# Kernel tuning notes

Hardware: AMD Instinct MI355X
Metric: run time of the kernel (lower is better)

## Reference

```python
import jax, jax.numpy as jnp
import numpy as np
from jax import lax

SR = 4      # sr_ratio
HEADS = 8   # num_heads


def _upsample_bilinear_ac(x, out_h, out_w):
    # torch nn.Upsample(scale_factor=SR, mode='bilinear', align_corners=True)
    B, C, h, w = x.shape
    ys = jnp.linspace(0.0, h - 1.0, out_h)
    xs = jnp.linspace(0.0, w - 1.0, out_w)
    y0 = jnp.floor(ys).astype(jnp.int32)
    y1 = jnp.minimum(y0 + 1, h - 1)
    wy = (ys - y0).astype(x.dtype)
    x0 = jnp.floor(xs).astype(jnp.int32)
    x1 = jnp.minimum(x0 + 1, w - 1)
    wx = (xs - x0).astype(x.dtype)
    r = x[:, :, y0, :] * (1.0 - wy)[None, None, :, None] + x[:, :, y1, :] * wy[None, None, :, None]
    return r[:, :, :, x0] * (1.0 - wx) + r[:, :, :, x1] * wx


def _forward(x, sr_w, sr_b, ln_g, ln_b, q_w, k1_w, v1_w, k2_w, v2_w, proj_w, proj_b):
    B, C, H, W = x.shape
    ID = C // 4                      # internal_dim
    hd = ID // HEADS                 # head_dim
    scale = float(hd) ** -0.5
    # spatial-reduction conv for Q path: [B, ID, H/4, W/4]
    qf = lax.conv_general_dilated(x, sr_w, (SR, SR), 'VALID',
                                  dimension_numbers=('NCHW', 'OIHW', 'NCHW'))
    qf = qf + sr_b[None, :, None, None]
    Hs, Ws = qf.shape[2], qf.shape[3]
    N = Hs * Ws
    qf = qf.reshape(B, ID, N).transpose(0, 2, 1)          # [B, N, ID]
    # LayerNorm
    mu = qf.mean(-1, keepdims=True)
    var = qf.var(-1, keepdims=True)
    qn = (qf - mu) / jnp.sqrt(var + 1e-5) * ln_g + ln_b
    q = qn @ q_w                                          # [B, N, ID]
    # max / avg pooled K,V inputs: [B, N, C]
    xm = lax.reduce_window(x, -jnp.inf, lax.max, (1, 1, SR, SR), (1, 1, SR, SR), 'VALID')
    xm = xm.reshape(B, C, N).transpose(0, 2, 1)
    xa = lax.reduce_window(x, 0.0, lax.add, (1, 1, SR, SR), (1, 1, SR, SR), 'VALID') / float(SR * SR)
    xa = xa.reshape(B, C, N).transpose(0, 2, 1)

    def heads(t):
        return t.reshape(B, N, HEADS, hd).transpose(0, 2, 1, 3)  # [B, H, N, hd]

    qh = heads(q)
    k1, v1 = heads(xm @ k1_w), heads(xm @ v1_w)
    k2, v2 = heads(xa @ k2_w), heads(xa @ v2_w)

    def attend(k, v):
        a = jax.nn.softmax(jnp.einsum('bhnd,bhmd->bhnm', qh, k) * scale, axis=-1)
        return jnp.einsum('bhnm,bhmd->bhnd', a, v)

    z = attend(k1, v1) + attend(k2, v2)                   # [B, H, N, hd]
    z = z.transpose(0, 2, 1, 3).reshape(B, N, ID)
    z = z @ proj_w + proj_b                               # [B, N, C]
    z = z.transpose(0, 2, 1).reshape(B, C, Hs, Ws)
    return _upsample_bilinear_ac(z, H, W)


def setup_inputs() -> dict:
    key = jax.random.key(0)
    ks = jax.random.split(key, 9)
    B, C, H, W = 16, 256, 112, 112
    ID = C // 4

    def n(k, shape, s=0.02):
        return jax.random.normal(k, shape, jnp.float32) * s

    return {
        'x': jax.random.normal(ks[0], (B, C, H, W), jnp.float32),
        'sr_w': n(ks[1], (ID, C, SR, SR)),
        'sr_b': jnp.zeros((ID,), jnp.float32),
        'ln_g': jnp.ones((ID,), jnp.float32),
        'ln_b': jnp.zeros((ID,), jnp.float32),
        'q_w': n(ks[2], (ID, ID)),
        'k1_w': n(ks[3], (C, ID)),
        'v1_w': n(ks[4], (C, ID)),
        'k2_w': n(ks[5], (C, ID)),
        'v2_w': n(ks[6], (C, ID)),
        'proj_w': n(ks[7], (ID, C)),
        'proj_b': jnp.zeros((C,), jnp.float32),
    }


def reference(x, sr_w, sr_b, ln_g, ln_b, q_w, k1_w, v1_w, k2_w, v2_w, proj_w, proj_b):
    return _forward(x, sr_w, sr_b, ln_g, ln_b, q_w, k1_w, v1_w, k2_w, v2_w, proj_w, proj_b)
```

## Files before the change

kernel.cpp:

```cpp
#include <hip/hip_runtime.h>
#include <math.h>

typedef __attribute__((ext_vector_type(8))) short short8;
typedef __attribute__((ext_vector_type(4))) short bh4;
typedef __attribute__((ext_vector_type(4))) float f32x4;
typedef __attribute__((ext_vector_type(2))) unsigned uint2v;
typedef __attribute__((ext_vector_type(4))) unsigned uint4v;

#define MFMA16(A,B,C) __builtin_amdgcn_mfma_f32_16x16x32_bf16(A,B,C,0,0,0)

#if __has_builtin(__builtin_amdgcn_mfma_f32_16x16x16bf16_1k)
#define MFMA16x16(A,B,C) __builtin_amdgcn_mfma_f32_16x16x16bf16_1k(A,B,C,0,0,0)
#else
__device__ __forceinline__ f32x4 mfma16x16_asm(bh4 a, bh4 b, f32x4 c){
    asm volatile("v_mfma_f32_16x16x16_bf16 %0, %1, %2, %0" : "+v"(c) : "v"(a), "v"(b));
    return c;
}
#define MFMA16x16(A,B,C) mfma16x16_asm(A,B,C)
#endif

__device__ __forceinline__ unsigned short f2b(float f){
    unsigned u = __builtin_bit_cast(unsigned, f);
    return (unsigned short)((u + 0x7fffu + ((u>>16)&1u)) >> 16);
}
__device__ __forceinline__ unsigned pk2(float a, float b){
    return (unsigned)f2b(a) | ((unsigned)f2b(b) << 16);
}
__device__ __forceinline__ unsigned pk2rn(float a, float b){
    unsigned ua = __builtin_bit_cast(unsigned, a) + 0x8000u;
    unsigned ub = __builtin_bit_cast(unsigned, b) + 0x8000u;
    return (ua >> 16) | (ub & 0xffff0000u);
}


__global__ __launch_bounds__(256) void ktw(const float* __restrict__ srw,
    const float* __restrict__ qw, const float* __restrict__ k1w,
    const float* __restrict__ v1w, const float* __restrict__ k2w,
    const float* __restrict__ v2w, char* __restrict__ srwb,
    char* __restrict__ Wtm, char* __restrict__ Wta, char* __restrict__ QWt)
{
    int blk = blockIdx.x, t = threadIdx.x;
    if (blk < 128){
        int base = blk*2048 + t*8;
        float4 a = *(const float4*)(srw + base);
        float4 b = *(const float4*)(srw + base + 4);
        uint4 u = { pk2(a.x,a.y), pk2(a.z,a.w), pk2(b.x,b.y), pk2(b.z,b.w) };
        *(uint4*)(srwb + (size_t)base*2) = u;
    } else if (blk < 136){
        __shared__ float T[256*33];
        int idx = blk - 128, fi = idx >> 1, half = idx & 1;
        const float* src = (fi==0) ? k1w : (fi==1) ? v1w : (fi==2) ? k2w : v2w;
        char* dst = ((fi < 2) ? Wtm : Wta) + (size_t)((fi & 1)*64 + half*32) * 512;
        for (int li = t; li < 8192; li += 256){
            int c = li >> 5, o = li & 31;
            T[c*33 + o] = src[c*64 + half*32 + o];
        }
        __syncthreads();
        for (int lo = t; lo < 1024; lo += 256){
            int o = lo >> 5, c8 = lo & 31;
            float v[8];
            #pragma unroll
            for (int k = 0; k < 8; ++k) v[k] = T[(c8*8 + k)*33 + o];
            uint4 u = { pk2(v[0],v[1]), pk2(v[2],v[3]), pk2(v[4],v[5]), pk2(v[6],v[7]) };
            *(uint4*)(dst + o*512 + c8*16) = u;
        }
    } else {
        __shared__ float T[64*65];
        for (int li = t; li < 4096; li += 256)
            T[(li >> 6)*65 + (li & 63)] = qw[li];
        __syncthreads();
        for (int lo = t; lo < 512; lo += 256){
            int o = lo >> 3, i8 = lo & 7;
            float v[8];
            #pragma unroll
            for (int k = 0; k < 8; ++k) v[k] = T[(i8*8 + k)*65 + o];
            uint4 u = { pk2(v[0],v[1]), pk2(v[2],v[3]), pk2(v[4],v[5]), pk2(v[6],v[7]) };
            *(uint4*)(QWt + o*128 + i8*16) = u;
        }
    }
}

__global__ __launch_bounds__(256) void k1(const float* __restrict__ x,
    const char* __restrict__ srwb, char* __restrict__ R, float* __restrict__ pws)
{
    __shared__ float pm[28*66];
    __shared__ float pa[28*66];
    int blk = blockIdx.x;
    int b = blk / 112, r5 = blk % 112, hs = r5 >> 2, cg4 = r5 & 3;
    int t = threadIdx.x;
    int w = t >> 6, l = t & 63, lr = l & 15, lg = l >> 4;
    int cpar = lg >> 1, r0 = (lg & 1) * 2;
    f32x4 acc0 = {0.f,0.f,0.f,0.f}, acc1 = {0.f,0.f,0.f,0.f};
    const float* xc = x + (size_t)(b*256 + cg4*64)*12544 + (size_t)(hs*4 + r0)*112;
    const char* Brow = srwb + (size_t)(w*16 + lr)*8192 + cg4*2048 + lg*16;
    int p0 = lr, p1 = min(16 + lr, 27);
    size_t rowB = (size_t)b*784 + hs*28;

    #pragma unroll 8
    for (int ks = 0; ks < 32; ++ks){
        const float* s = xc + (size_t)(ks*2 + cpar)*12544;
        float4 a0r0 = *(const float4*)(s + p0*4);
        float4 a0r1 = *(const float4*)(s + 112 + p0*4);
        float4 a1r0 = *(const float4*)(s + p1*4);
        float4 a1r1 = *(const float4*)(s + 112 + p1*4);
        short8 bf = *(const short8*)(Brow + ks*64);
        if (w == 0){
            float mx0 = fmaxf(fmaxf(fmaxf(a0r0.x,a0r0.y),fmaxf(a0r0.z,a0r0.w)),
                              fmaxf(fmaxf(a0r1.x,a0r1.y),fmaxf(a0r1.z,a0r1.w)));
            float sm0 = (a0r0.x+a0r0.y)+(a0r0.z+a0r0.w)+(a0r1.x+a0r1.y)+(a0r1.z+a0r1.w);
            float mx1 = fmaxf(fmaxf(fmaxf(a1r0.x,a1r0.y),fmaxf(a1r0.z,a1r0.w)),
                              fmaxf(fmaxf(a1r1.x,a1r1.y),fmaxf(a1r1.z,a1r1.w)));
            float sm1 = (a1r0.x+a1r0.y)+(a1r0.z+a1r0.w)+(a1r1.x+a1r1.y)+(a1r1.z+a1r1.w);
            mx0 = fmaxf(mx0, __shfl_xor(mx0, 16, 64));
            sm0 = sm0 + __shfl_xor(sm0, 16, 64);
            mx1 = fmaxf(mx1, __shfl_xor(mx1, 16, 64));
            sm1 = sm1 + __shfl_xor(sm1, 16, 64);
            if ((lg & 1) == 0){
                int c = ks*2 + cpar;
                pm[p0*66 + c] = mx0; pa[p0*66 + c] = sm0 * (1.f/16.f);
                if (lr < 12){ pm[p1*66 + c] = mx1; pa[p1*66 + c] = sm1 * (1.f/16.f); }
            }
        }
        short8 af0 = __builtin_bit_cast(short8,
            (uint4v){ pk2(a0r0.x,a0r0.y), pk2(a0r0.z,a0r0.w), pk2(a0r1.x,a0r1.y), pk2(a0r1.z,a0r1.w) });
        short8 af1 = __builtin_bit_cast(short8,
            (uint4v){ pk2(a1r0.x,a1r0.y), pk2(a1r0.z,a1r0.w), pk2(a1r1.x,a1r1.y), pk2(a1r1.z,a1r1.w) });
        acc0 = MFMA16(af0, bf, acc0);
        acc1 = MFMA16(af1, bf, acc1);
    }

    float* pp = pws + (size_t)((b*28 + hs)*4 + cg4)*1792;
    #pragma unroll
    for (int rg = 0; rg < 4; ++rg){
        int m0 = lg*4 + rg, m1 = 16 + lg*4 + rg;
        pp[m0*64 + w*16 + lr] = acc0[rg];
        if (m1 < 28) pp[m1*64 + w*16 + lr] = acc1[rg];
    }
    __syncthreads();
    if (t < 224){
        int m = t >> 3, sub = t & 7;
        float vm[8], va8[8];
        #pragma unroll
        for (int k = 0; k < 8; ++k){
            vm[k]  = pm[m*66 + sub*8 + k];
            va8[k] = pa[m*66 + sub*8 + k];
        }
        uint4 um = { pk2(vm[0],vm[1]), pk2(vm[2],vm[3]), pk2(vm[4],vm[5]), pk2(vm[6],vm[7]) };
        uint4 ua = { pk2(va8[0],va8[1]), pk2(va8[2],va8[3]), pk2(va8[4],va8[5]), pk2(va8[6],va8[7]) };
        *(uint4*)(R + (rowB + m)*1024 + cg4*128 + sub*16)       = um;
        *(uint4*)(R + (rowB + m)*1024 + 512 + cg4*128 + sub*16) = ua;
    }
}

__global__ __launch_bounds__(512) void k2(const float* __restrict__ pws_,
    const float* __restrict__ srb, const float* __restrict__ lng,
    const float* __restrict__ lnb, const char* __restrict__ Wtm,
    const char* __restrict__ Wta, const char* __restrict__ QWt,
    char* __restrict__ R)
{
    __shared__ __align__(16) char PM[16384];
    __shared__ __align__(16) char PA[16384];
    __shared__ float Db[32*64];
    __shared__ __align__(16) char QN[4096];
    int blk = blockIdx.x, b = blk/28, hs = blk%28;
    int t = threadIdx.x, w = t>>6, l = t&63, lr = l&15, lg = l>>4;
    size_t rowB = (size_t)b*784 + hs*28;
    const char* Rb = R + rowB*1024;
    for (int li = t; li < 896; li += 512){
        int m = li >> 5, c16 = li & 31;
        uint4 vm = *(const uint4*)(Rb + (size_t)m*1024 + c16*16);
        uint4 va = *(const uint4*)(Rb + (size_t)m*1024 + 512 + c16*16);
        int dst = m*512 + ((c16*16) ^ ((m&7)<<4));
        *(uint4*)(PM + dst) = vm;
        *(uint4*)(PA + dst) = va;
    }
    const float* p0 = pws_ + (size_t)(b*28 + hs)*4*1792;
    for (int e = t; e < 1792; e += 512)
        Db[e] = ((p0[e] + p0[1792+e]) + (p0[3584+e] + p0[5376+e])) + srb[e & 63];
    __syncthreads();
    float g = lng[l], be = lnb[l];
    #pragma unroll
    for (int i = 0; i < 4; ++i){
        int m = w + i*8;
        float v = Db[m*64 + l];
        float s = v, ss = v*v;
        #pragma unroll
        for (int off = 1; off < 64; off <<= 1){
            s  += __shfl_xor(s,  off, 64);
            ss += __shfl_xor(ss, off, 64);
        }
        float mu = s * (1.f/64.f);
        float var = ss * (1.f/64.f) - mu*mu;
        float qn = (v - mu) * rsqrtf(var + 1e-5f) * g + be;
        *(unsigned short*)(QN + m*128 + ((l*2) ^ ((m&7)<<4))) = f2b(qn);
    }
    __syncthreads();
    int fam = w >> 2, ofp = w & 3;
    const char* PMA = fam ? PA : PM;
    const char* Wt  = fam ? Wta : Wtm;
    f32x4 a00={0.f,0.f,0.f,0.f}, a01=a00, a10=a00, a11=a00;
    int swzr = (lr & 7) << 4;
    #pragma unroll
    for (int ks = 0; ks < 8; ++ks){
        int kb = ks*64 + lg*16;
        short8 x0 = *(const short8*)(PMA + lr*512 + (kb ^ swzr));
        short8 x1 = *(const short8*)(PMA + (16+lr)*512 + (kb ^ swzr));
        short8 b0 = *(const short8*)(Wt + (size_t)(ofp*32 + lr)*512 + kb);
        short8 b1 = *(const short8*)(Wt + (size_t)(ofp*32 + 16 + lr)*512 + kb);
        a00 = MFMA16(x0, b0, a00); a01 = MFMA16(x0, b1, a01);
        a10 = MFMA16(x1, b0, a10); a11 = MFMA16(x1, b1, a11);
    }
    f32x4 q0={0.f,0.f,0.f,0.f}, q1=q0;
    if (w < 4){
        #pragma unroll
        for (int ks = 0; ks < 2; ++ks){
            int kb = ks*64 + lg*16;
            short8 xa_ = *(const short8*)(QN + lr*128 + (kb ^ swzr));
            short8 xb_ = *(const short8*)(QN + (16+lr)*128 + (kb ^ swzr));
            short8 bq  = *(const short8*)(QWt + (size_t)(w*16 + lr)*128 + kb);
            q0 = MFMA16(xa_, bq, q0);
            q1 = MFMA16(xb_, bq, q1);
        }
    }
    #pragma unroll
    for (int j = 0; j < 2; ++j){
        int o128 = ofp*32 + j*16 + lr;
        int o = o128 & 63, hh = o >> 3, dd = o & 7, mat = fam*2 + (o128 >> 6);
        int byteoff = 128 + hh*64 + mat*16 + dd*2;
        f32x4 am  = j ? a01 : a00;
        f32x4 am1 = j ? a11 : a10;
        #pragma unroll
        for (int rg = 0; rg < 4; ++rg){
            int m0 = lg*4 + rg, m1 = 16 + lg*4 + rg;
            *(unsigned short*)(R + (rowB + m0)*1024 + byteoff) = f2b(am[rg]);
            if (m1 < 28)
                *(unsigned short*)(R + (rowB + m1)*1024 + byteoff) = f2b(am1[rg]);
        }
    }
    if (w < 4){
        int o = w*16 + lr;
        #pragma unroll
        for (int rg = 0; rg < 4; ++rg){
            int m0 = lg*4 + rg, m1 = 16 + lg*4 + rg;
            *(unsigned short*)(R + (rowB + m0)*1024 + o*2) = f2b(q0[rg]);
            if (m1 < 28)
                *(unsigned short*)(R + (rowB + m1)*1024 + o*2) = f2b(q1[rg]);
        }
    }
}

__global__ __launch_bounds__(256) void kattn(const char* __restrict__ R, float* __restrict__ z)
{
    __shared__ __align__(16) char QT [6144];
    __shared__ __align__(16) char K1b[5376];
    __shared__ __align__(16) char K2b[5376];
    __shared__ __align__(16) char VT1[3840];
    __shared__ __align__(16) char VT2[3840];
    int blk = blockIdx.x;
    int bh = blk / 7, nseg = blk % 7;
    int b = bh >> 3, h = bh & 7;
    int t = threadIdx.x, w = t >> 6, l = t & 63;
    int col = l & 15, g = l >> 4;

    for (int i = t; i < 384; i += 256) ((uint4*)QT)[i] = uint4{0,0,0,0};
    for (int i = t; i < 112; i += 256){
        *(uint4*)(K1b + i*48 + 16) = uint4{0,0,0,0};
        *(uint4*)(K2b + i*48 + 16) = uint4{0,0,0,0};
    }
    for (int i = t; i < 120; i += 256){
        *(uint4*)(VT1 + 1920 + i*16) = uint4{0,0,0,0};
        *(uint4*)(VT2 + 1920 + i*16) = uint4{0,0,0,0};
    }
    __syncthreads();
    if (t < 112){
        uint4 qv = *(const uint4*)(R + ((size_t)b*784 + nseg*112 + t)*1024 + h*16);
        *(uint2*)(QT + t*48)     = uint2{qv.x, qv.y};
        *(uint2*)(QT + t*48 + 8) = uint2{qv.z, qv.w};
    }
    __syncthreads();

    bh4 qf[2];
    #pragma unroll
    for (int nf = 0; nf < 2; ++nf)
        qf[nf] = *(const bh4*)(QT + (w*28 + nf*16 + col)*48 + g*8);

    f32x4 o1[2] = {{0,0,0,0},{0,0,0,0}}, o2[2] = {{0,0,0,0},{0,0,0,0}};
    float d1[2] = {0.f,0.f}, d2[2] = {0.f,0.f};
    const float C2 = 0.51004244f;

    for (int mt = 0; mt < 7; ++mt){
        __syncthreads();
        for (int li = t; li < 448; li += 256){
            int m = li >> 2, part = li & 3;
            uint4 v = *(const uint4*)(R + ((size_t)b*784 + mt*112 + m)*1024 + 128 + h*64 + part*16);
            if ((part & 1) == 0){
                char* Kb = (part == 0) ? K1b : K2b;
                *(uint2*)(Kb + m*48)     = uint2{v.x, v.y};
                *(uint2*)(Kb + m*48 + 8) = uint2{v.z, v.w};
            } else {
                char* Vb = (part == 1) ? VT1 : VT2;
                unsigned arr[4] = {v.x, v.y, v.z, v.w};
                #pragma unroll
                for (int d = 0; d < 4; ++d){
                    *(unsigned short*)(Vb + (d*2)*240   + m*2) = (unsigned short)(arr[d] & 0xffffu);
                    *(unsigned short*)(Vb + (d*2+1)*240 + m*2) = (unsigned short)(arr[d] >> 16);
                }
            }
        }
        __syncthreads();
        #pragma unroll
        for (int mc = 0; mc < 7; ++mc){
            bh4 ka = *(const bh4*)(K1b + (mc*16 + col)*48 + g*8);
            bh4 kb = *(const bh4*)(K2b + (mc*16 + col)*48 + g*8);
            bh4 va = *(const bh4*)(VT1 + col*240 + mc*32 + g*8);
            bh4 vb = *(const bh4*)(VT2 + col*240 + mc*32 + g*8);
            #pragma unroll
            for (int nf = 0; nf < 2; ++nf){
                f32x4 zr = {0.f,0.f,0.f,0.f};
                f32x4 s1 = MFMA16x16(ka, qf[nf], zr);
                float p0 = exp2f(s1[0]*C2), p1 = exp2f(s1[1]*C2);
                float p2 = exp2f(s1[2]*C2), p3 = exp2f(s1[3]*C2);
                d1[nf] += (p0+p1)+(p2+p3);
                bh4 pf1 = __builtin_bit_cast(bh4, (uint2v){pk2rn(p0,p1), pk2rn(p2,p3)});
                o1[nf] = MFMA16x16(va, pf1, o1[nf]);
                f32x4 s2 = MFMA16x16(kb, qf[nf], zr);
                float r0 = exp2f(s2[0]*C2), r1 = exp2f(s2[1]*C2);
                float r2 = exp2f(s2[2]*C2), r3 = exp2f(s2[3]*C2);
                d2[nf] += (r0+r1)+(r2+r3);
                bh4 pf2 = __builtin_bit_cast(bh4, (uint2v){pk2rn(r0,r1), pk2rn(r2,r3)});
                o2[nf] = MFMA16x16(vb, pf2, o2[nf]);
            }
        }
    }
    #pragma unroll
    for (int nf = 0; nf < 2; ++nf){
        d1[nf] += __shfl_xor(d1[nf], 16, 64); d1[nf] += __shfl_xor(d1[nf], 32, 64);
        d2[nf] += __shfl_xor(d2[nf], 16, 64); d2[nf] += __shfl_xor(d2[nf], 32, 64);
    }
    if (g < 2){
        #pragma unroll
        for (int nf = 0; nf < 2; ++nf){
            if (nf == 1 && col >= 12) continue;
            int n = nseg*112 + w*28 + nf*16 + col;
            float ra = 1.f / d1[nf], rb = 1.f / d2[nf];
            float4 ov;
            ov.x = o1[nf][0]*ra + o2[nf][0]*rb;
            ov.y = o1[nf][1]*ra + o2[nf][1]*rb;
            ov.z = o1[nf][2]*ra + o2[nf][2]*rb;
            ov.w = o1[nf][3]*ra + o2[nf][3]*rb;
            *(float4*)(z + ((size_t)b*784 + n)*64 + h*8 + g*4) = ov;
        }
    }
}

__global__ __launch_bounds__(256) void kproj(const float* __restrict__ z,
    const float* __restrict__ pw, const float* __restrict__ pb,
    float* __restrict__ zc)
{
    __shared__ float zs[28*64];
    int blk = blockIdx.x;
    int b = blk / 28, hs = blk % 28;
    int t = threadIdx.x;
    const float* zrow = z + ((size_t)b*784 + hs*28)*64;
    for (int li = t; li < 1792; li += 256) zs[li] = zrow[li];
    __syncthreads();
    int c = t;
    float acc[28];
    float bias = pb[c];
    #pragma unroll
    for (int wsI = 0; wsI < 28; ++wsI) acc[wsI] = bias;
    for (int o = 0; o < 64; ++o){
        float wv = pw[o*256 + c];
        #pragma unroll
        for (int wsI = 0; wsI < 28; ++wsI) acc[wsI] = fmaf(zs[wsI*64+o], wv, acc[wsI]);
    }
    float* op = zc + (((size_t)(b*256 + c))*28 + hs)*28;
    #pragma unroll
    for (int f = 0; f < 7; ++f)
        ((float4*)op)[f] = make_float4(acc[4*f], acc[4*f+1], acc[4*f+2], acc[4*f+3]);
}

__global__ __launch_bounds__(256) void kups(const float* __restrict__ zc, float* __restrict__ out)
{
    __shared__ float plane[784];
    __shared__ int   ti0[112];
    __shared__ float twv[112];
    int bc = blockIdx.x;
    int t = threadIdx.x;
    const float* src = zc + (size_t)bc*784;
    for (int li = t; li < 784; li += 256) plane[li] = src[li];
    if (t < 112){
        float s = (float)t * (27.f/111.f);
        int i0 = (int)s;
        if (i0 > 27) i0 = 27;
        ti0[t] = i0;
        twv[t] = s - (float)i0;
    }
    __syncthreads();
    float* op = out + (size_t)bc*12544;
    for (int i = t; i < 12544; i += 256){
        int y = i/112, xx = i%112;
        int y0 = ti0[y], x0 = ti0[xx];
        float wy = twv[y], wx = twv[xx];
        int y1 = min(y0+1, 27), x1 = min(x0+1, 27);
        const float* r0 = plane + y0*28;
        const float* r1 = plane + y1*28;
        float a  = r0[x0] + (r1[x0]-r0[x0])*wy;
        float bb = r0[x1] + (r1[x1]-r0[x1])*wy;
        op[i] = a + (bb-a)*wx;
    }
}

extern "C" void kernel_launch(void* const* d_in, const int* in_sizes, int n_in,
                              void* d_out, int out_size, void* d_ws, size_t ws_size,
                              hipStream_t stream) {
    const float* x   = (const float*)d_in[0];
    const float* srw = (const float*)d_in[1];
    const float* srb = (const float*)d_in[2];
    const float* lng = (const float*)d_in[3];
    const float* lnb = (const float*)d_in[4];
    const float* qw  = (const float*)d_in[5];
    const float* k1w = (const float*)d_in[6];
    const float* v1w = (const float*)d_in[7];
    const float* k2w = (const float*)d_in[8];
    const float* v2w = (const float*)d_in[9];
    const float* pw  = (const float*)d_in[10];
    const float* pb  = (const float*)d_in[11];

    char*  Rws  = (char*)d_ws;
    float* pws  = (float*)(Rws + 12845056);
    char*  srwb = Rws + 25690112;
    char*  Wtm  = Rws + 26214400;
    char*  Wta  = Rws + 26279936;
    char*  QWt  = Rws + 26345472;
    float* z    = (float*)(Rws + 12845056);
    float* zc   = (float*)(Rws + 16056320);
    float* out  = (float*)d_out;

    ktw  <<<137,  256, 0, stream>>>(srw, qw, k1w, v1w, k2w, v2w, srwb, Wtm, Wta, QWt);
    k1   <<<1792, 256, 0, stream>>>(x, srwb, Rws, pws);
    k2   <<<448,  512, 0, stream>>>(pws, srb, lng, lnb, Wtm, Wta, QWt, Rws);
    kattn<<<896,  256, 0, stream>>>(Rws, z);
    kproj<<<448,  256, 0, stream>>>(z, pw, pb, zc);
    kups <<<4096, 256, 0, stream>>>(zc, out);
}
```

Before: 284.4 us.

## Fuse projection with bilinear upsample and software-pipeline k1 loads

Merges the output projection and the bilinear upsample into one kernel. Each block computes 8 channel planes of one batch in shared memory and upsamples them directly to the output, so the intermediate zc buffer is never written to or read back from global memory. Separately, k1's channel loop is double-buffered by hand, loading the next two channel pairs while processing the current ones, and gets a launch-bounds occupancy hint. The cost is more registers in k1 and only 512 blocks for the fused kernel, each of which re-reads z.

```diff
diff --git a/kernel.cpp b/kernel.cpp
--- a/kernel.cpp
+++ b/kernel.cpp
@@ -80,7 +80,7 @@
     }
 }
 
-__global__ __launch_bounds__(256) void k1(const float* __restrict__ x,
+__global__ __launch_bounds__(256, 4) void k1(const float* __restrict__ x,
     const char* __restrict__ srwb, char* __restrict__ R, float* __restrict__ pws)
 {
     __shared__ float pm[28*66];
@@ -96,38 +96,56 @@
     int p0 = lr, p1 = min(16 + lr, 27);
     size_t rowB = (size_t)b*784 + hs*28;
 
-    #pragma unroll 8
-    for (int ks = 0; ks < 32; ++ks){
-        const float* s = xc + (size_t)(ks*2 + cpar)*12544;
-        float4 a0r0 = *(const float4*)(s + p0*4);
-        float4 a0r1 = *(const float4*)(s + 112 + p0*4);
-        float4 a1r0 = *(const float4*)(s + p1*4);
-        float4 a1r1 = *(const float4*)(s + 112 + p1*4);
-        short8 bf = *(const short8*)(Brow + ks*64);
-        if (w == 0){
-            float mx0 = fmaxf(fmaxf(fmaxf(a0r0.x,a0r0.y),fmaxf(a0r0.z,a0r0.w)),
-                              fmaxf(fmaxf(a0r1.x,a0r1.y),fmaxf(a0r1.z,a0r1.w)));
-            float sm0 = (a0r0.x+a0r0.y)+(a0r0.z+a0r0.w)+(a0r1.x+a0r1.y)+(a0r1.z+a0r1.w);
-            float mx1 = fmaxf(fmaxf(fmaxf(a1r0.x,a1r0.y),fmaxf(a1r0.z,a1r0.w)),
-                              fmaxf(fmaxf(a1r1.x,a1r1.y),fmaxf(a1r1.z,a1r1.w)));
-            float sm1 = (a1r0.x+a1r0.y)+(a1r0.z+a1r0.w)+(a1r1.x+a1r1.y)+(a1r1.z+a1r1.w);
-            mx0 = fmaxf(mx0, __shfl_xor(mx0, 16, 64));
-            sm0 = sm0 + __shfl_xor(sm0, 16, 64);
-            mx1 = fmaxf(mx1, __shfl_xor(mx1, 16, 64));
-            sm1 = sm1 + __shfl_xor(sm1, 16, 64);
-            if ((lg & 1) == 0){
-                int c = ks*2 + cpar;
-                pm[p0*66 + c] = mx0; pa[p0*66 + c] = sm0 * (1.f/16.f);
-                if (lr < 12){ pm[p1*66 + c] = mx1; pa[p1*66 + c] = sm1 * (1.f/16.f); }
-            }
-        }
-        short8 af0 = __builtin_bit_cast(short8,
-            (uint4v){ pk2(a0r0.x,a0r0.y), pk2(a0r0.z,a0r0.w), pk2(a0r1.x,a0r1.y), pk2(a0r1.z,a0r1.w) });
-        short8 af1 = __builtin_bit_cast(short8,
-            (uint4v){ pk2(a1r0.x,a1r0.y), pk2(a1r0.z,a1r0.w), pk2(a1r1.x,a1r1.y), pk2(a1r1.z,a1r1.w) });
-        acc0 = MFMA16(af0, bf, acc0);
-        acc1 = MFMA16(af1, bf, acc1);
-    }
+    float4 XA0,XA1,XA2,XA3,XA4,XA5,XA6,XA7; short8 BA0,BA1;
+    float4 XB0,XB1,XB2,XB3,XB4,XB5,XB6,XB7; short8 BB0,BB1;
+
+#define LD2(X0,X1,X2,X3,X4,X5,X6,X7,Bq0,Bq1,KS) do{ \
+    const float* _s0 = xc + (size_t)((KS)*2 + cpar)*12544; \
+    const float* _s1 = xc + (size_t)(((KS)+1)*2 + cpar)*12544; \
+    X0=*(const float4*)(_s0+p0*4); X1=*(const float4*)(_s0+112+p0*4); \
+    X2=*(const float4*)(_s0+p1*4); X3=*(const float4*)(_s0+112+p1*4); \
+    X4=*(const float4*)(_s1+p0*4); X5=*(const float4*)(_s1+112+p0*4); \
+    X6=*(const float4*)(_s1+p1*4); X7=*(const float4*)(_s1+112+p1*4); \
+    Bq0=*(const short8*)(Brow+(KS)*64); Bq1=*(const short8*)(Brow+((KS)+1)*64); }while(0)
+
+#define PROC1(Y0,Y1,Y2,Y3,BF,KS) do{ \
+    if (w == 0){ \
+        float mx0 = fmaxf(fmaxf(fmaxf(Y0.x,Y0.y),fmaxf(Y0.z,Y0.w)), \
+                          fmaxf(fmaxf(Y1.x,Y1.y),fmaxf(Y1.z,Y1.w))); \
+        float sm0 = (Y0.x+Y0.y)+(Y0.z+Y0.w)+(Y1.x+Y1.y)+(Y1.z+Y1.w); \
+        float mx1 = fmaxf(fmaxf(fmaxf(Y2.x,Y2.y),fmaxf(Y2.z,Y2.w)), \
+                          fmaxf(fmaxf(Y3.x,Y3.y),fmaxf(Y3.z,Y3.w))); \
+        float sm1 = (Y2.x+Y2.y)+(Y2.z+Y2.w)+(Y3.x+Y3.y)+(Y3.z+Y3.w); \
+        mx0 = fmaxf(mx0, __shfl_xor(mx0, 16, 64)); \
+        sm0 = sm0 + __shfl_xor(sm0, 16, 64); \
+        mx1 = fmaxf(mx1, __shfl_xor(mx1, 16, 64)); \
+        sm1 = sm1 + __shfl_xor(sm1, 16, 64); \
+        if ((lg & 1) == 0){ \
+            int c = (KS)*2 + cpar; \
+            pm[p0*66 + c] = mx0; pa[p0*66 + c] = sm0 * (1.f/16.f); \
+            if (lr < 12){ pm[p1*66 + c] = mx1; pa[p1*66 + c] = sm1 * (1.f/16.f); } \
+        } \
+    } \
+    short8 af0 = __builtin_bit_cast(short8, \
+        (uint4v){ pk2(Y0.x,Y0.y), pk2(Y0.z,Y0.w), pk2(Y1.x,Y1.y), pk2(Y1.z,Y1.w) }); \
+    short8 af1 = __builtin_bit_cast(short8, \
+        (uint4v){ pk2(Y2.x,Y2.y), pk2(Y2.z,Y2.w), pk2(Y3.x,Y3.y), pk2(Y3.z,Y3.w) }); \
+    acc0 = MFMA16(af0, BF, acc0); \
+    acc1 = MFMA16(af1, BF, acc1); }while(0)
+
+    LD2(XA0,XA1,XA2,XA3,XA4,XA5,XA6,XA7,BA0,BA1, 0);
+    #pragma unroll
+    for (int s2 = 0; s2 < 8; ++s2){
+        int ka = s2*4;
+        LD2(XB0,XB1,XB2,XB3,XB4,XB5,XB6,XB7,BB0,BB1, ka+2);
+        PROC1(XA0,XA1,XA2,XA3,BA0, ka);
+        PROC1(XA4,XA5,XA6,XA7,BA1, ka+1);
+        if (s2 < 7) LD2(XA0,XA1,XA2,XA3,XA4,XA5,XA6,XA7,BA0,BA1, ka+4);
+        PROC1(XB0,XB1,XB2,XB3,BB0, ka+2);
+        PROC1(XB4,XB5,XB6,XB7,BB1, ka+3);
+    }
+#undef LD2
+#undef PROC1
 
     float* pp = pws + (size_t)((b*28 + hs)*4 + cg4)*1792;
     #pragma unroll
@@ -353,61 +371,71 @@
     }
 }
 
-__global__ __launch_bounds__(256) void kproj(const float* __restrict__ z,
+__global__ __launch_bounds__(256) void kpu(const float* __restrict__ z,
     const float* __restrict__ pw, const float* __restrict__ pb,
-    float* __restrict__ zc)
+    float* __restrict__ out)
 {
-    __shared__ float zs[28*64];
-    int blk = blockIdx.x;
-    int b = blk / 28, hs = blk % 28;
-    int t = threadIdx.x;
-    const float* zrow = z + ((size_t)b*784 + hs*28)*64;
-    for (int li = t; li < 1792; li += 256) zs[li] = zrow[li];
-    __syncthreads();
-    int c = t;
-    float acc[28];
-    float bias = pb[c];
-    #pragma unroll
-    for (int wsI = 0; wsI < 28; ++wsI) acc[wsI] = bias;
-    for (int o = 0; o < 64; ++o){
-        float wv = pw[o*256 + c];
-        #pragma unroll
-        for (int wsI = 0; wsI < 28; ++wsI) acc[wsI] = fmaf(zs[wsI*64+o], wv, acc[wsI]);
-    }
-    float* op = zc + (((size_t)(b*256 + c))*28 + hs)*28;
-    #pragma unroll
-    for (int f = 0; f < 7; ++f)
-        ((float4*)op)[f] = make_float4(acc[4*f], acc[4*f+1], acc[4*f+2], acc[4*f+3]);
-}
-
-__global__ __launch_bounds__(256) void kups(const float* __restrict__ zc, float* __restrict__ out)
-{
-    __shared__ float plane[784];
+    __shared__ float plane[8*784];
+    __shared__ float wsl[64*8];
     __shared__ int   ti0[112];
     __shared__ float twv[112];
-    int bc = blockIdx.x;
+    int blk = blockIdx.x;
+    int b = blk >> 5, cg = blk & 31;
     int t = threadIdx.x;
-    const float* src = zc + (size_t)bc*784;
-    for (int li = t; li < 784; li += 256) plane[li] = src[li];
+    if (t < 128){
+        #pragma unroll
+        for (int q = 0; q < 4; ++q){
+            int idx = t*4 + q; int o = idx >> 3, j = idx & 7;
+            wsl[o*8 + j] = pw[o*256 + cg*8 + j];
+        }
+    }
     if (t < 112){
         float s = (float)t * (27.f/111.f);
-        int i0 = (int)s;
-        if (i0 > 27) i0 = 27;
-        ti0[t] = i0;
-        twv[t] = s - (float)i0;
-    }
-    __syncthreads();
-    float* op = out + (size_t)bc*12544;
+        int i0 = (int)s; if (i0 > 27) i0 = 27;
+        ti0[t] = i0; twv[t] = s - (float)i0;
+    }
+    __syncthreads();
+    {
+        int nh = t >> 1, jh = (t & 1) * 4;
+        float bias0 = pb[cg*8 + jh], bias1 = pb[cg*8 + jh + 1];
+        float bias2 = pb[cg*8 + jh + 2], bias3 = pb[cg*8 + jh + 3];
+        for (int n = nh; n < 784; n += 128){
+            const float* zr = z + ((size_t)b*784 + n)*64;
+            float a0 = bias0, a1 = bias1, a2 = bias2, a3 = bias3;
+            #pragma unroll
+            for (int o4 = 0; o4 < 16; ++o4){
+                float4 zv = *(const float4*)(zr + o4*4);
+                const float* wr = wsl + (o4*4)*8 + jh;
+                a0 = fmaf(zv.x, wr[0],  a0); a1 = fmaf(zv.x, wr[1],  a1);
+                a2 = fmaf(zv.x, wr[2],  a2); a3 = fmaf(zv.x, wr[3],  a3);
+                a0 = fmaf(zv.y, wr[8],  a0); a1 = fmaf(zv.y, wr[9],  a1);
+                a2 = fmaf(zv.y, wr[10], a2); a3 = fmaf(zv.y, wr[11], a3);
+                a0 = fmaf(zv.z, wr[16], a0); a1 = fmaf(zv.z, wr[17], a1);
+                a2 = fmaf(zv.z, wr[18], a2); a3 = fmaf(zv.z, wr[19], a3);
+                a0 = fmaf(zv.w, wr[24], a0); a1 = fmaf(zv.w, wr[25], a1);
+                a2 = fmaf(zv.w, wr[26], a2); a3 = fmaf(zv.w, wr[27], a3);
+            }
+            plane[(jh+0)*784 + n] = a0;
+            plane[(jh+1)*784 + n] = a1;
+            plane[(jh+2)*784 + n] = a2;
+            plane[(jh+3)*784 + n] = a3;
+        }
+    }
+    __syncthreads();
+    float* ob = out + ((size_t)b*256 + cg*8)*12544;
     for (int i = t; i < 12544; i += 256){
         int y = i/112, xx = i%112;
         int y0 = ti0[y], x0 = ti0[xx];
         float wy = twv[y], wx = twv[xx];
         int y1 = min(y0+1, 27), x1 = min(x0+1, 27);
-        const float* r0 = plane + y0*28;
-        const float* r1 = plane + y1*28;
-        float a  = r0[x0] + (r1[x0]-r0[x0])*wy;
-        float bb = r0[x1] + (r1[x1]-r0[x1])*wy;
-        op[i] = a + (bb-a)*wx;
+        int i00 = y0*28 + x0, i01 = y0*28 + x1, i10 = y1*28 + x0, i11 = y1*28 + x1;
+        #pragma unroll
+        for (int j = 0; j < 8; ++j){
+            const float* pl = plane + j*784;
+            float a  = pl[i00] + (pl[i10]-pl[i00])*wy;
+            float bb = pl[i01] + (pl[i11]-pl[i01])*wy;
+            ob[(size_t)j*12544 + i] = a + (bb-a)*wx;
+        }
     }
 }
 
@@ -434,13 +462,11 @@
     char*  Wta  = Rws + 26279936;
     char*  QWt  = Rws + 26345472;
     float* z    = (float*)(Rws + 12845056);
-    float* zc   = (float*)(Rws + 16056320);
     float* out  = (float*)d_out;
 
     ktw  <<<137,  256, 0, stream>>>(srw, qw, k1w, v1w, k2w, v2w, srwb, Wtm, Wta, QWt);
     k1   <<<1792, 256, 0, stream>>>(x, srwb, Rws, pws);
     k2   <<<448,  512, 0, stream>>>(pws, srb, lng, lnb, Wtm, Wta, QWt, Rws);
     kattn<<<896,  256, 0, stream>>>(Rws, z);
-    kproj<<<448,  256, 0, stream>>>(z, pw, pb, zc);
-    kups <<<4096, 256, 0, stream>>>(zc, out);
-}
+    kpu  <<<512,  256, 0, stream>>>(z, pw, pb, out);
+}
```

Result: faster. 258.2 us (-9.2%).
